# Kernel tuning notes

Measured on AMD Instinct MI355X. Metric: run time of the kernel, lower is better.

The kernel has to match this reference:

```python
import jax, jax.numpy as jnp
import numpy as np
from jax import lax


def setup_inputs() -> dict:
    key = jax.random.key(0)
    k1, k2, k3, k4 = jax.random.split(key, 4)
    D = 128
    B = 16
    image = jax.random.normal(k1, (1, D, D, D), jnp.float32)          # [1, D, H, W]
    x = jax.random.normal(k2, (B, 1, D, D, D), jnp.float32)           # [B, 1, D, H, W]
    # Conv3d(1, 27, kernel_size=3) parameters
    W = jax.random.normal(k3, (27, 1, 3, 3, 3), jnp.float32) * (1.0 / np.sqrt(27.0))
    b = jax.random.normal(k4, (27,), jnp.float32) * 0.01
    return {"image": image, "x": x, "W": W, "b": b}


def reference(image, x, W, b):
    D, H, Wd = image.shape[1], image.shape[2], image.shape[3]
    # K = Conv3d(image): per-voxel 27 filter taps. Unbatched CDHW -> add batch dim.
    K = lax.conv_general_dilated(
        image[None], W, window_strides=(1, 1, 1), padding='SAME',
        dimension_numbers=('NCDHW', 'OIDHW', 'NCDHW'))[0]             # [27, D, H, W]
    K = K + b[:, None, None, None]
    # permute (1,2,3,0) + unflatten(3,(3,3,3)) -> [D, H, W, 3, 3, 3]
    K = jnp.moveaxis(K, 0, -1).reshape(D, H, Wd, 3, 3, 3)
    # Apply dynamic per-voxel 3x3x3 filter: sum of 27 shifted slices
    xp = jnp.pad(x, ((0, 0), (0, 0), (1, 1), (1, 1), (1, 1)))         # [B,1,D+2,H+2,W+2]
    y = jnp.zeros_like(x)
    for di in range(3):
        for dj in range(3):
            for dk in range(3):
                tap = K[..., di, dj, dk][None, None]                  # [1,1,D,H,W]
                y = y + tap * xp[:, :, di:di + D, dj:dj + H, dk:dk + Wd]
    return y
```

## Files before the change

### kernel.cpp

```cpp
#include <hip/hip_runtime.h>

typedef __fp16 f16x2 __attribute__((ext_vector_type(2)));

#define Dm 128
#define Bn 16
#define TZ 4
#define TYt 8
#define TXv 16
#define HZ 6
#define HY 10
#define HX 18
#define HXP 24
#define TILE_A 1536
#define NT 256
#define NLOAD (TILE_A / NT)
#define VOX (Dm * Dm * Dm)
#define BCH 2
#define NCH (Bn / BCH)

__device__ __forceinline__ void gload_lds4(const void* g, void* l) {
  __builtin_amdgcn_global_load_lds(
      (const __attribute__((address_space(1))) void*)g,
      (__attribute__((address_space(3))) void*)l,
      4, 0, 0);
}
__device__ __forceinline__ int iclamp(int v, int lo, int hi) {
  return v < lo ? lo : (v > hi ? hi : v);
}
__device__ __forceinline__ f16x2 pkrtz(float lo, float hi) {
  return __builtin_amdgcn_cvt_pkrtz(lo, hi);
}
__device__ __forceinline__ f16x2 midpair(f16x2 h23, f16x2 h01) {
  unsigned r = __builtin_amdgcn_perm(__builtin_bit_cast(unsigned, h23),
                                     __builtin_bit_cast(unsigned, h01),
                                     0x05040302u);
  return __builtin_bit_cast(f16x2, r);
}

extern "C" __global__ void __launch_bounds__(NT, 4)
fused3d(const float* __restrict__ img, const float* __restrict__ x,
        const float* __restrict__ Wf, const float* __restrict__ bfp,
        float* __restrict__ out)
{
  __shared__ float sImg[TILE_A];
  __shared__ float sX[2][BCH][TILE_A];

  const int tid = threadIdx.x;
  const int tx = tid & 7;
  const int ty = (tid >> 3) & 7;
  const int tz = tid >> 6;

  const int bid = blockIdx.x;
  const int s  = (bid & 7) * 512 + (bid >> 3);
  const int bx = s & 7, by = (s >> 3) & 15, bz = s >> 7;
  const int w0 = bx * TXv, h0 = by * TYt, d0 = bz * TZ;

  int goff[NLOAD]; bool gin[NLOAD];
#pragma unroll
  for (int k = 0; k < NLOAD; ++k) {
    int i  = tid + k * NT;
    int r  = i / HXP;
    int c  = i - r * HXP;
    int zz = r / HY;
    int yy = r - zz * HY;
    int gd = d0 + zz - 1, gh = h0 + yy - 1, gw = w0 + c - 1;
    gin[k]  = (zz < HZ) & (c < HX) &
              ((unsigned)gd < Dm) & ((unsigned)gh < Dm) & ((unsigned)gw < Dm);
    goff[k] = (iclamp(gd, 0, Dm - 1) * Dm + iclamp(gh, 0, Dm - 1)) * Dm
              + iclamp(gw, 0, Dm - 1);
  }

#pragma unroll
  for (int k = 0; k < NLOAD; ++k) sImg[tid + k * NT] = 0.f;
  __syncthreads();

  const int wbase = tid & ~63;
#pragma unroll
  for (int k = 0; k < NLOAD; ++k)
    if (gin[k]) gload_lds4(img + goff[k], &sImg[k * NT + wbase]);
#pragma unroll
  for (int j = 0; j < BCH; ++j) {
    const float* xb = x + (size_t)j * VOX;
#pragma unroll
    for (int k = 0; k < NLOAD; ++k)
      gload_lds4(xb + goff[k], &sX[0][j][k * NT + wbase]);
  }
  __syncthreads();

  const int od = d0 + tz, oh = h0 + ty, ow = w0 + 2 * tx;
  const int tbase = (tz * HY + ty) * HXP + 2 * tx;

  f16x2 K2[27];
#pragma unroll
  for (int oc = 0; oc < 9; ++oc) {
    float a0[3], a1[3];
#pragma unroll
    for (int q = 0; q < 3; ++q) { float bb = bfp[oc * 3 + q]; a0[q] = bb; a1[q] = bb; }
#pragma unroll
    for (int rr = 0; rr < 9; ++rr) {
      const int base = tbase + ((rr / 3) * HY + (rr % 3)) * HXP;
      float2 a  = *(const float2*)&sImg[base];
      float2 b2 = *(const float2*)&sImg[base + 2];
#pragma unroll
      for (int q = 0; q < 3; ++q) {
        const int o = oc * 3 + q;
        const float wa = Wf[o * 27 + rr * 3 + 0];
        const float wb = Wf[o * 27 + rr * 3 + 1];
        const float wc = Wf[o * 27 + rr * 3 + 2];
        a0[q] = fmaf(wa, a.x, fmaf(wb, a.y,  fmaf(wc, b2.x, a0[q])));
        a1[q] = fmaf(wa, a.y, fmaf(wb, b2.x, fmaf(wc, b2.y, a1[q])));
      }
    }
#pragma unroll
    for (int q = 0; q < 3; ++q) {
      const int o = oc * 3 + q;
      const int di = o / 9, dj = (o / 3) % 3, dk = o % 3;
      const bool mm = ((unsigned)(od + di - 1) < Dm) & ((unsigned)(oh + dj - 1) < Dm);
      const float m0 = (mm & ((unsigned)(ow + dk - 1) < Dm)) ? 1.f : 0.f;
      const float m1 = (mm & ((unsigned)(ow + dk)     < Dm)) ? 1.f : 0.f;
      K2[o] = pkrtz(a0[q] * m0, a1[q] * m1);
    }
  }

  const size_t obase = (((size_t)od) * Dm + oh) * Dm + ow;

  for (int ch = 0; ch < NCH; ++ch) {
    const int cur = ch & 1;
    if (ch + 1 < NCH) {
      const float* xc = x + (size_t)(ch + 1) * BCH * VOX;
#pragma unroll
      for (int j = 0; j < BCH; ++j) {
        const float* xb = xc + (size_t)j * VOX;
#pragma unroll
        for (int k = 0; k < NLOAD; ++k)
          gload_lds4(xb + goff[k], &sX[cur ^ 1][j][k * NT + wbase]);
      }
    }

#pragma unroll
    for (int j = 0; j < BCH; ++j) {
      const float* sxb = sX[cur][j];
      f16x2 accA = {(__fp16)0.f, (__fp16)0.f};
      f16x2 accB = {(__fp16)0.f, (__fp16)0.f};
#pragma unroll
      for (int rr = 0; rr < 9; ++rr) {
        const int base = tbase + ((rr / 3) * HY + (rr % 3)) * HXP;
        float2 a  = *(const float2*)&sxb[base];
        float2 b2 = *(const float2*)&sxb[base + 2];
        f16x2 h01 = pkrtz(a.x, a.y);
        f16x2 h23 = pkrtz(b2.x, b2.y);
        f16x2 h12 = midpair(h23, h01);
        if (rr & 1) {
          accB = __builtin_elementwise_fma(K2[rr * 3 + 0], h01, accB);
          accB = __builtin_elementwise_fma(K2[rr * 3 + 1], h12, accB);
          accB = __builtin_elementwise_fma(K2[rr * 3 + 2], h23, accB);
        } else {
          accA = __builtin_elementwise_fma(K2[rr * 3 + 0], h01, accA);
          accA = __builtin_elementwise_fma(K2[rr * 3 + 1], h12, accA);
          accA = __builtin_elementwise_fma(K2[rr * 3 + 2], h23, accA);
        }
      }
      f16x2 acc = accA + accB;
      float2 st; st.x = (float)acc.x; st.y = (float)acc.y;
      *(float2*)&out[(size_t)(ch * BCH + j) * VOX + obase] = st;
    }

    __syncthreads();
  }
}

extern "C" void kernel_launch(void* const* d_in, const int* in_sizes, int n_in,
                              void* d_out, int out_size, void* d_ws, size_t ws_size,
                              hipStream_t stream) {
  const float* img = (const float*)d_in[0];
  const float* x   = (const float*)d_in[1];
  const float* Wf  = (const float*)d_in[2];
  const float* bf  = (const float*)d_in[3];
  float* out = (float*)d_out;
  hipLaunchKernelGGL(fused3d, dim3(4096), dim3(NT), 0, stream, img, x, Wf, bf, out);
}
```

Before: 121.1 us.

## Stage x and image tiles as packed fp16 pairs in LDS via register prefetch

Replaces the direct global-to-LDS fp32 loads with register loads that convert pairs of voxels to packed fp16 before storing them to LDS. This halves the LDS footprint and the LDS read traffic, and removes the per-tap conversions in the inner loop. The weight-generating conv now runs in packed fp16 FMAs, using weights pre-packed by a small extra kernel. Double buffering in LDS is replaced by register prefetch plus an extra barrier per chunk, and computing the conv in fp16 adds precision risk.

```diff
diff --git a/kernel.cpp b/kernel.cpp
--- a/kernel.cpp
+++ b/kernel.cpp
@@ -7,28 +7,26 @@
 #define TZ 4
 #define TYt 8
 #define TXv 16
-#define HZ 6
 #define HY 10
-#define HX 18
-#define HXP 24
-#define TILE_A 1536
+#define WPR 12
+#define TILE_W 768
 #define NT 256
-#define NLOAD (TILE_A / NT)
+#define NPAIR 3
 #define VOX (Dm * Dm * Dm)
 #define BCH 2
 #define NCH (Bn / BCH)
 
-__device__ __forceinline__ void gload_lds4(const void* g, void* l) {
-  __builtin_amdgcn_global_load_lds(
-      (const __attribute__((address_space(1))) void*)g,
-      (__attribute__((address_space(3))) void*)l,
-      4, 0, 0);
-}
 __device__ __forceinline__ int iclamp(int v, int lo, int hi) {
   return v < lo ? lo : (v > hi ? hi : v);
 }
 __device__ __forceinline__ f16x2 pkrtz(float lo, float hi) {
   return __builtin_amdgcn_cvt_pkrtz(lo, hi);
+}
+__device__ __forceinline__ float pkbits(float lo, float hi) {
+  return __builtin_bit_cast(float, __builtin_amdgcn_cvt_pkrtz(lo, hi));
+}
+__device__ __forceinline__ f16x2 asf16x2(float w) {
+  return __builtin_bit_cast(f16x2, w);
 }
 __device__ __forceinline__ f16x2 midpair(f16x2 h23, f16x2 h01) {
   unsigned r = __builtin_amdgcn_perm(__builtin_bit_cast(unsigned, h23),
@@ -37,13 +35,20 @@
   return __builtin_bit_cast(f16x2, r);
 }
 
+extern "C" __global__ void packW(const float* __restrict__ Wf,
+                                 const float* __restrict__ bfp,
+                                 float* __restrict__ wpk) {
+  int i = blockIdx.x * 256 + threadIdx.x;
+  if (i < 729)       wpk[i] = pkbits(Wf[i], Wf[i]);
+  else if (i < 756)  { float b = bfp[i - 729]; wpk[i] = pkbits(b, b); }
+}
+
 extern "C" __global__ void __launch_bounds__(NT, 4)
 fused3d(const float* __restrict__ img, const float* __restrict__ x,
-        const float* __restrict__ Wf, const float* __restrict__ bfp,
-        float* __restrict__ out)
+        const float* __restrict__ wpk, float* __restrict__ out)
 {
-  __shared__ float sImg[TILE_A];
-  __shared__ float sX[2][BCH][TILE_A];
+  __shared__ float sImgP[TILE_W];
+  __shared__ float sXP[BCH][TILE_W];
 
   const int tid = threadIdx.x;
   const int tx = tid & 7;
@@ -55,116 +60,123 @@
   const int bx = s & 7, by = (s >> 3) & 15, bz = s >> 7;
   const int w0 = bx * TXv, h0 = by * TYt, d0 = bz * TZ;
 
-  int goff[NLOAD]; bool gin[NLOAD];
+  int off0[NPAIR], off1[NPAIR];
+  float oki0[NPAIR], oki1[NPAIR];
 #pragma unroll
-  for (int k = 0; k < NLOAD; ++k) {
-    int i  = tid + k * NT;
-    int r  = i / HXP;
-    int c  = i - r * HXP;
+  for (int k = 0; k < NPAIR; ++k) {
+    int p  = k * NT + tid;
+    int r  = p / WPR;
+    int c  = 2 * (p - r * WPR);
     int zz = r / HY;
     int yy = r - zz * HY;
-    int gd = d0 + zz - 1, gh = h0 + yy - 1, gw = w0 + c - 1;
-    gin[k]  = (zz < HZ) & (c < HX) &
-              ((unsigned)gd < Dm) & ((unsigned)gh < Dm) & ((unsigned)gw < Dm);
-    goff[k] = (iclamp(gd, 0, Dm - 1) * Dm + iclamp(gh, 0, Dm - 1)) * Dm
-              + iclamp(gw, 0, Dm - 1);
+    int gd = d0 + zz - 1, gh = h0 + yy - 1;
+    int g0 = w0 + c - 1,  g1 = w0 + c;
+    int base = (iclamp(gd, 0, Dm - 1) * Dm + iclamp(gh, 0, Dm - 1)) * Dm;
+    off0[k] = base + iclamp(g0, 0, Dm - 1);
+    off1[k] = base + iclamp(g1, 0, Dm - 1);
+    bool rk = ((unsigned)gd < Dm) & ((unsigned)gh < Dm);
+    oki0[k] = (rk & ((unsigned)g0 < Dm)) ? 1.f : 0.f;
+    oki1[k] = (rk & ((unsigned)g1 < Dm)) ? 1.f : 0.f;
   }
 
+  float ri0[NPAIR], ri1[NPAIR], rx0[BCH][NPAIR], rx1[BCH][NPAIR];
 #pragma unroll
-  for (int k = 0; k < NLOAD; ++k) sImg[tid + k * NT] = 0.f;
+  for (int k = 0; k < NPAIR; ++k) {
+    ri0[k] = img[off0[k]] * oki0[k];
+    ri1[k] = img[off1[k]] * oki1[k];
+  }
+#pragma unroll
+  for (int j = 0; j < BCH; ++j)
+#pragma unroll
+    for (int k = 0; k < NPAIR; ++k) {
+      rx0[j][k] = x[(size_t)j * VOX + off0[k]];
+      rx1[j][k] = x[(size_t)j * VOX + off1[k]];
+    }
+#pragma unroll
+  for (int k = 0; k < NPAIR; ++k)
+    sImgP[k * NT + tid] = pkbits(ri0[k], ri1[k]);
+#pragma unroll
+  for (int j = 0; j < BCH; ++j)
+#pragma unroll
+    for (int k = 0; k < NPAIR; ++k)
+      sXP[j][k * NT + tid] = pkbits(rx0[j][k], rx1[j][k]);
   __syncthreads();
 
-  const int wbase = tid & ~63;
+  const int tbase = (tz * HY + ty) * WPR + tx;
+  f16x2 K2[27];
 #pragma unroll
-  for (int k = 0; k < NLOAD; ++k)
-    if (gin[k]) gload_lds4(img + goff[k], &sImg[k * NT + wbase]);
+  for (int o = 0; o < 27; ++o) K2[o] = asf16x2(wpk[729 + o]);
 #pragma unroll
-  for (int j = 0; j < BCH; ++j) {
-    const float* xb = x + (size_t)j * VOX;
+  for (int rr = 0; rr < 9; ++rr) {
+    const int wofs = tbase + ((rr / 3) * HY + (rr % 3)) * WPR;
+    float u0 = sImgP[wofs], u1 = sImgP[wofs + 1];
+    f16x2 h01 = asf16x2(u0), h23 = asf16x2(u1), h12 = midpair(h23, h01);
 #pragma unroll
-    for (int k = 0; k < NLOAD; ++k)
-      gload_lds4(xb + goff[k], &sX[0][j][k * NT + wbase]);
+    for (int o = 0; o < 27; ++o) {
+      K2[o] = __builtin_elementwise_fma(asf16x2(wpk[o * 27 + rr * 3 + 0]), h01, K2[o]);
+      K2[o] = __builtin_elementwise_fma(asf16x2(wpk[o * 27 + rr * 3 + 1]), h12, K2[o]);
+      K2[o] = __builtin_elementwise_fma(asf16x2(wpk[o * 27 + rr * 3 + 2]), h23, K2[o]);
+    }
   }
-  __syncthreads();
 
   const int od = d0 + tz, oh = h0 + ty, ow = w0 + 2 * tx;
-  const int tbase = (tz * HY + ty) * HXP + 2 * tx;
-
-  f16x2 K2[27];
 #pragma unroll
-  for (int oc = 0; oc < 9; ++oc) {
-    float a0[3], a1[3];
-#pragma unroll
-    for (int q = 0; q < 3; ++q) { float bb = bfp[oc * 3 + q]; a0[q] = bb; a1[q] = bb; }
-#pragma unroll
-    for (int rr = 0; rr < 9; ++rr) {
-      const int base = tbase + ((rr / 3) * HY + (rr % 3)) * HXP;
-      float2 a  = *(const float2*)&sImg[base];
-      float2 b2 = *(const float2*)&sImg[base + 2];
-#pragma unroll
-      for (int q = 0; q < 3; ++q) {
-        const int o = oc * 3 + q;
-        const float wa = Wf[o * 27 + rr * 3 + 0];
-        const float wb = Wf[o * 27 + rr * 3 + 1];
-        const float wc = Wf[o * 27 + rr * 3 + 2];
-        a0[q] = fmaf(wa, a.x, fmaf(wb, a.y,  fmaf(wc, b2.x, a0[q])));
-        a1[q] = fmaf(wa, a.y, fmaf(wb, b2.x, fmaf(wc, b2.y, a1[q])));
-      }
-    }
-#pragma unroll
-    for (int q = 0; q < 3; ++q) {
-      const int o = oc * 3 + q;
-      const int di = o / 9, dj = (o / 3) % 3, dk = o % 3;
-      const bool mm = ((unsigned)(od + di - 1) < Dm) & ((unsigned)(oh + dj - 1) < Dm);
-      const float m0 = (mm & ((unsigned)(ow + dk - 1) < Dm)) ? 1.f : 0.f;
-      const float m1 = (mm & ((unsigned)(ow + dk)     < Dm)) ? 1.f : 0.f;
-      K2[o] = pkrtz(a0[q] * m0, a1[q] * m1);
-    }
+  for (int o = 0; o < 27; ++o) {
+    const int di = o / 9, dj = (o / 3) % 3, dk = o % 3;
+    const bool mm = ((unsigned)(od + di - 1) < Dm) & ((unsigned)(oh + dj - 1) < Dm);
+    const float m0 = (mm & ((unsigned)(ow + dk - 1) < Dm)) ? 1.f : 0.f;
+    const float m1 = (mm & ((unsigned)(ow + dk)     < Dm)) ? 1.f : 0.f;
+    K2[o] *= pkrtz(m0, m1);
   }
 
   const size_t obase = (((size_t)od) * Dm + oh) * Dm + ow;
 
+  float nx0[BCH][NPAIR], nx1[BCH][NPAIR];
   for (int ch = 0; ch < NCH; ++ch) {
-    const int cur = ch & 1;
     if (ch + 1 < NCH) {
       const float* xc = x + (size_t)(ch + 1) * BCH * VOX;
 #pragma unroll
-      for (int j = 0; j < BCH; ++j) {
-        const float* xb = xc + (size_t)j * VOX;
+      for (int j = 0; j < BCH; ++j)
 #pragma unroll
-        for (int k = 0; k < NLOAD; ++k)
-          gload_lds4(xb + goff[k], &sX[cur ^ 1][j][k * NT + wbase]);
-      }
+        for (int k = 0; k < NPAIR; ++k) {
+          nx0[j][k] = xc[(size_t)j * VOX + off0[k]];
+          nx1[j][k] = xc[(size_t)j * VOX + off1[k]];
+        }
     }
 
 #pragma unroll
     for (int j = 0; j < BCH; ++j) {
-      const float* sxb = sX[cur][j];
-      f16x2 accA = {(__fp16)0.f, (__fp16)0.f};
-      f16x2 accB = {(__fp16)0.f, (__fp16)0.f};
+      const float* sx = sXP[j];
+      f16x2 aA = {(__fp16)0.f, (__fp16)0.f};
+      f16x2 aB = {(__fp16)0.f, (__fp16)0.f};
 #pragma unroll
       for (int rr = 0; rr < 9; ++rr) {
-        const int base = tbase + ((rr / 3) * HY + (rr % 3)) * HXP;
-        float2 a  = *(const float2*)&sxb[base];
-        float2 b2 = *(const float2*)&sxb[base + 2];
-        f16x2 h01 = pkrtz(a.x, a.y);
-        f16x2 h23 = pkrtz(b2.x, b2.y);
-        f16x2 h12 = midpair(h23, h01);
+        const int wofs = tbase + ((rr / 3) * HY + (rr % 3)) * WPR;
+        float u0 = sx[wofs], u1 = sx[wofs + 1];
+        f16x2 h01 = asf16x2(u0), h23 = asf16x2(u1), h12 = midpair(h23, h01);
         if (rr & 1) {
-          accB = __builtin_elementwise_fma(K2[rr * 3 + 0], h01, accB);
-          accB = __builtin_elementwise_fma(K2[rr * 3 + 1], h12, accB);
-          accB = __builtin_elementwise_fma(K2[rr * 3 + 2], h23, accB);
+          aB = __builtin_elementwise_fma(K2[rr * 3 + 0], h01, aB);
+          aB = __builtin_elementwise_fma(K2[rr * 3 + 1], h12, aB);
+          aB = __builtin_elementwise_fma(K2[rr * 3 + 2], h23, aB);
         } else {
-          accA = __builtin_elementwise_fma(K2[rr * 3 + 0], h01, accA);
-          accA = __builtin_elementwise_fma(K2[rr * 3 + 1], h12, accA);
-          accA = __builtin_elementwise_fma(K2[rr * 3 + 2], h23, accA);
+          aA = __builtin_elementwise_fma(K2[rr * 3 + 0], h01, aA);
+          aA = __builtin_elementwise_fma(K2[rr * 3 + 1], h12, aA);
+          aA = __builtin_elementwise_fma(K2[rr * 3 + 2], h23, aA);
         }
       }
-      f16x2 acc = accA + accB;
+      f16x2 acc = aA + aB;
       float2 st; st.x = (float)acc.x; st.y = (float)acc.y;
       *(float2*)&out[(size_t)(ch * BCH + j) * VOX + obase] = st;
     }
 
+    __syncthreads();
+    if (ch + 1 < NCH) {
+#pragma unroll
+      for (int j = 0; j < BCH; ++j)
+#pragma unroll
+        for (int k = 0; k < NPAIR; ++k)
+          sXP[j][k * NT + tid] = pkbits(nx0[j][k], nx1[j][k]);
+    }
     __syncthreads();
   }
 }
@@ -177,5 +189,7 @@
   const float* Wf  = (const float*)d_in[2];
   const float* bf  = (const float*)d_in[3];
   float* out = (float*)d_out;
-  hipLaunchKernelGGL(fused3d, dim3(4096), dim3(NT), 0, stream, img, x, Wf, bf, out);
+  float* wpk = (float*)d_ws;
+  hipLaunchKernelGGL(packW, dim3(3), dim3(256), 0, stream, Wf, bf, wpk);
+  hipLaunchKernelGGL(fused3d, dim3(4096), dim3(256), 0, stream, img, x, wpk, out);
 }
```

After: 130.6 us. 1.08x slower.
